# Kernel optimization log

Measured on AMD Instinct MI355X. Metric: run time of the kernel, lower is better.

## Reference

```python
import jax, jax.numpy as jnp
import numpy as np

DIM = 1024
HEAD_NUM = 8
D_HEAD = DIM // HEAD_NUM
B, S = 4, 2048


def setup_inputs() -> dict:
    key = jax.random.key(0)
    ks = jax.random.split(key, 7)
    scale = 0.02
    return {
        "Q": jax.random.normal(ks[0], (B, S, DIM), dtype=jnp.float32),
        "K": jax.random.normal(ks[1], (B, S, DIM), dtype=jnp.float32),
        "V": jax.random.normal(ks[2], (B, S, DIM), dtype=jnp.float32),
        "W_Q": jax.random.normal(ks[3], (DIM, DIM), dtype=jnp.float32) * scale,
        "W_K": jax.random.normal(ks[4], (DIM, DIM), dtype=jnp.float32) * scale,
        "W_V": jax.random.normal(ks[5], (DIM, DIM), dtype=jnp.float32) * scale,
        "W_O": jax.random.normal(ks[6], (DIM, DIM), dtype=jnp.float32) * scale,
    }


def reference(Q, K, V, W_Q, W_K, W_V, W_O):
    # torch nn.Linear(bias=False): y = x @ W.T
    b, s, d = Q.shape
    h, dh = HEAD_NUM, d // HEAD_NUM

    def proj_split(x, W):
        # split_head: tensor_split along feature dim into h contiguous chunks,
        # stack at dim 1 -> [b, h, s, dh]; equivalent to reshape+transpose.
        y = jnp.einsum('bsd,ed->bse', x, W)
        return y.reshape(b, s, h, dh).transpose(0, 2, 1, 3)

    q = proj_split(Q, W_Q)  # [b,h,s,dh]
    k = proj_split(K, W_K)
    v = proj_split(V, W_V)

    scores = jnp.einsum('bhqd,bhkd->bhqk', q, k) / jnp.sqrt(jnp.float32(dh))
    # FAITHFUL to original: nn.Softmax(dim=1) normalizes over the HEAD axis.
    attn = jax.nn.softmax(scores, axis=1)
    # dropout is identity in eval mode
    ctx = jnp.einsum('bhqk,bhkd->bhqd', attn, v)  # [b,h,s,dh]
    # concat_head: heads concatenated back along feature dim in order
    ctx = ctx.transpose(0, 2, 1, 3).reshape(b, s, d)
    return jnp.einsum('bsd,ed->bse', ctx, W_O)
```

## Files before the change

kernel.cpp:

```cpp
#include <hip/hip_runtime.h>
#include <math.h>
#include <stdint.h>


typedef __attribute__((ext_vector_type(8))) __bf16 bf16x8;
typedef __attribute__((ext_vector_type(4))) __bf16 bf16x4;
typedef __attribute__((ext_vector_type(4))) float  f32x4;

__device__ __forceinline__ f32x4 mfma16(bf16x8 a, bf16x8 b, f32x4 c) {
    return __builtin_amdgcn_mfma_f32_16x16x32_bf16(a, b, c, 0, 0, 0);
}

__device__ __forceinline__ void cp16(void* lds, const void* g) {
    __builtin_amdgcn_global_load_lds(
        (__attribute__((address_space(1))) void*)(void*)(const_cast<void*>(g)),
        (__attribute__((address_space(3))) void*)lds,
        16, 0, 0);
}

__global__ void cast4_f32_to_bf16(const float* __restrict__ s0, __bf16* __restrict__ d0,
                                  const float* __restrict__ s1, __bf16* __restrict__ d1,
                                  const float* __restrict__ s2, __bf16* __restrict__ d2,
                                  const float* __restrict__ s3, __bf16* __restrict__ d3,
                                  int n4) {
    const float* s = (blockIdx.y == 0) ? s0 : (blockIdx.y == 1) ? s1
                    : (blockIdx.y == 2) ? s2 : s3;
    __bf16* d = (blockIdx.y == 0) ? d0 : (blockIdx.y == 1) ? d1
               : (blockIdx.y == 2) ? d2 : d3;
    int i = blockIdx.x * blockDim.x + threadIdx.x;
    const int stride = gridDim.x * blockDim.x;
    for (; i < n4; i += stride) {
        float4 f = ((const float4*)s)[i];
        bf16x4 o;
        o[0] = (__bf16)f.x; o[1] = (__bf16)f.y; o[2] = (__bf16)f.z; o[3] = (__bf16)f.w;
        ((bf16x4*)d)[i] = o;
    }
}

__global__ void cast3_f32_to_bf16(const float* __restrict__ s0, __bf16* __restrict__ d0,
                                  const float* __restrict__ s1, __bf16* __restrict__ d1,
                                  const float* __restrict__ s2, __bf16* __restrict__ d2,
                                  int n4) {
    const float* s = (blockIdx.y == 0) ? s0 : (blockIdx.y == 1) ? s1 : s2;
    __bf16* d = (blockIdx.y == 0) ? d0 : (blockIdx.y == 1) ? d1 : d2;
    int i = blockIdx.x * blockDim.x + threadIdx.x;
    const int stride = gridDim.x * blockDim.x;
    for (; i < n4; i += stride) {
        float4 f = ((const float4*)s)[i];
        bf16x4 o;
        o[0] = (__bf16)f.x; o[1] = (__bf16)f.y; o[2] = (__bf16)f.z; o[3] = (__bf16)f.w;
        ((bf16x4*)d)[i] = o;
    }
}

template<int MODE>
__global__ __launch_bounds__(256, 2) void gemm_bt(const __bf16* __restrict__ A,
                                                  const __bf16* __restrict__ Bt,
                                                  void* __restrict__ out,
                                                  float scale)
{
    __shared__ __bf16 As[128 * 32];
    __shared__ __bf16 Bs[128 * 32];
    const int tid  = threadIdx.x;
    const int lane = tid & 63;
    const int u = lane >> 4, v = lane & 15;
    const int w = tid >> 6;
    const int wm = (w >> 1) * 64, wn = (w & 1) * 64;
    const long tM = (long)blockIdx.y * 128;
    const int  tN = blockIdx.x * 128;

    f32x4 acc[4][4];
#pragma unroll
    for (int i = 0; i < 4; ++i)
#pragma unroll
        for (int j = 0; j < 4; ++j) acc[i][j] = (f32x4){0.f, 0.f, 0.f, 0.f};

    const int c0 = tid, c1 = tid + 256;
    const int ar0 = c0 >> 2, ak0 = (c0 & 3) * 8;
    const int ar1 = c1 >> 2, ak1 = (c1 & 3) * 8;

    const __bf16* Ab = A  + tM * 1024;
    const __bf16* Bb = Bt + (long)tN * 1024;

    for (int k0 = 0; k0 < 1024; k0 += 32) {
        __syncthreads();
        cp16(&As[ar0 * 32 + ak0], Ab + (long)ar0 * 1024 + k0 + ak0);
        cp16(&As[ar1 * 32 + ak1], Ab + (long)ar1 * 1024 + k0 + ak1);
        cp16(&Bs[ar0 * 32 + ak0], Bb + (long)ar0 * 1024 + k0 + ak0);
        cp16(&Bs[ar1 * 32 + ak1], Bb + (long)ar1 * 1024 + k0 + ak1);
        __syncthreads();

        bf16x8 af[4], bfr[4];
#pragma unroll
        for (int i = 0; i < 4; ++i)
            af[i] = *(const bf16x8*)&As[(wm + i * 16 + v) * 32 + u * 8];
#pragma unroll
        for (int j = 0; j < 4; ++j)
            bfr[j] = *(const bf16x8*)&Bs[(wn + j * 16 + v) * 32 + u * 8];
#pragma unroll
        for (int i = 0; i < 4; ++i)
#pragma unroll
            for (int j = 0; j < 4; ++j)
                acc[i][j] = mfma16(af[i], bfr[j], acc[i][j]);
    }

#pragma unroll
    for (int i = 0; i < 4; ++i) {
#pragma unroll
        for (int j = 0; j < 4; ++j) {
            const long row0 = tM + wm + i * 16 + u * 4;
            const int  col  = tN + wn + j * 16 + v;
            if (MODE == 1) {
                float* o = (float*)out;
#pragma unroll
                for (int r = 0; r < 4; ++r)
                    o[(row0 + r) * 1024 + col] = acc[i][j][r];
            } else {
                __bf16* o = (__bf16*)out;
#pragma unroll
                for (int r = 0; r < 4; ++r)
                    o[(row0 + r) * 1024 + col] = (__bf16)(acc[i][j][r] * scale);
            }
        }
    }
}

__global__ __launch_bounds__(256, 2) void qkv_proj(
    const __bf16* __restrict__ xq, const __bf16* __restrict__ xk,
    const __bf16* __restrict__ xv,
    const __bf16* __restrict__ wq, const __bf16* __restrict__ wk,
    const __bf16* __restrict__ wv,
    __bf16* __restrict__ qp, __bf16* __restrict__ kp, __bf16* __restrict__ vtb,
    float qscale)
{
    __shared__ __bf16 As[128 * 32];
    __shared__ __bf16 Bs[128 * 32];
    const int z = blockIdx.z;
    const __bf16* A  = (z == 0) ? xq : (z == 1) ? xk : xv;
    const __bf16* Bt = (z == 0) ? wq : (z == 1) ? wk : wv;
    __bf16* out      = (z == 0) ? qp : (z == 1) ? kp : vtb;
    const float scale = (z == 0) ? qscale : 1.0f;

    const int tid  = threadIdx.x;
    const int lane = tid & 63;
    const int u = lane >> 4, v = lane & 15;
    const int w = tid >> 6;
    const int wm = (w >> 1) * 64, wn = (w & 1) * 64;
    const long tM = (long)blockIdx.y * 128;
    const int  tN = blockIdx.x * 128;

    f32x4 acc[4][4];
#pragma unroll
    for (int i = 0; i < 4; ++i)
#pragma unroll
        for (int j = 0; j < 4; ++j) acc[i][j] = (f32x4){0.f, 0.f, 0.f, 0.f};

    const int c0 = tid, c1 = tid + 256;
    const int ar0 = c0 >> 2, ak0 = (c0 & 3) * 8;
    const int ar1 = c1 >> 2, ak1 = (c1 & 3) * 8;

    const __bf16* Ab = A  + tM * 1024;
    const __bf16* Bb = Bt + (long)tN * 1024;

    for (int k0 = 0; k0 < 1024; k0 += 32) {
        __syncthreads();
        cp16(&As[ar0 * 32 + ak0], Ab + (long)ar0 * 1024 + k0 + ak0);
        cp16(&As[ar1 * 32 + ak1], Ab + (long)ar1 * 1024 + k0 + ak1);
        cp16(&Bs[ar0 * 32 + ak0], Bb + (long)ar0 * 1024 + k0 + ak0);
        cp16(&Bs[ar1 * 32 + ak1], Bb + (long)ar1 * 1024 + k0 + ak1);
        __syncthreads();

        bf16x8 af[4], bfr[4];
#pragma unroll
        for (int i = 0; i < 4; ++i)
            af[i] = *(const bf16x8*)&As[(wm + i * 16 + v) * 32 + u * 8];
#pragma unroll
        for (int j = 0; j < 4; ++j)
            bfr[j] = *(const bf16x8*)&Bs[(wn + j * 16 + v) * 32 + u * 8];
#pragma unroll
        for (int i = 0; i < 4; ++i)
#pragma unroll
            for (int j = 0; j < 4; ++j)
                acc[i][j] = mfma16(af[i], bfr[j], acc[i][j]);
    }

#pragma unroll
    for (int i = 0; i < 4; ++i) {
#pragma unroll
        for (int j = 0; j < 4; ++j) {
            const long row0 = tM + wm + i * 16 + u * 4;
            const int  col  = tN + wn + j * 16 + v;
            if (z < 2) {
#pragma unroll
                for (int r = 0; r < 4; ++r)
                    out[(row0 + r) * 1024 + col] = (__bf16)(acc[i][j][r] * scale);
            } else {
                const int bidx = (int)(row0 >> 11);
                const int s    = (int)(row0 & 2047);
                const int h = col >> 7, dh = col & 127;
                bf16x4 pk;
#pragma unroll
                for (int r = 0; r < 4; ++r) pk[r] = (__bf16)acc[i][j][r];
                *(bf16x4*)&out[((long)(bidx * 8 + h) * 128 + dh) * 2048 + s] = pk;
            }
        }
    }
}

__global__ __launch_bounds__(512, 2) void fused_attn(
    const __bf16* __restrict__ qp, const __bf16* __restrict__ kp,
    const __bf16* __restrict__ vt, __bf16* __restrict__ ctx)
{
    __shared__ f32x4 dbuf[8][8][64];
    __shared__ f32x4 rbuf[8][64];
    __shared__ __bf16 Pl[8][32][64];

    const int tid  = threadIdx.x;
    const int w    = tid >> 6;
    const int lane = tid & 63;
    const int u = lane >> 4, v = lane & 15;

    const int g0 = blockIdx.x;
    const int xs = g0 & 7, idx = g0 >> 3;
    const int b  = xs >> 1;
    const int qt = idx * 2 + (xs & 1);
    const int q0 = qt * 32;
    const int h  = w;

    const __bf16* Qb = qp + ((long)b * 2048 + q0) * 1024 + h * 128;
    const __bf16* Kb = kp + (long)b * 2048 * 1024 + h * 128;
    const __bf16* Vb = vt + (long)(b * 8 + h) * 128 * 2048;

    bf16x8 qf[2][4];
#pragma unroll
    for (int qj = 0; qj < 2; ++qj)
#pragma unroll
        for (int kk = 0; kk < 4; ++kk)
            qf[qj][kk] = *(const bf16x8*)&Qb[(long)(qj * 16 + v) * 1024 + kk * 32 + u * 8];

    f32x4 ctxa[8][2];
#pragma unroll
    for (int dt = 0; dt < 8; ++dt)
#pragma unroll
        for (int qj = 0; qj < 2; ++qj) ctxa[dt][qj] = (f32x4){0.f, 0.f, 0.f, 0.f};

    for (int kt = 0; kt < 2048; kt += 64) {
        f32x4 e[4][2];
#pragma unroll
        for (int ki = 0; ki < 4; ++ki)
#pragma unroll
            for (int qj = 0; qj < 2; ++qj) e[ki][qj] = (f32x4){0.f, 0.f, 0.f, 0.f};

#pragma unroll
        for (int ki = 0; ki < 4; ++ki) {
            bf16x8 kf[4];
#pragma unroll
            for (int kk = 0; kk < 4; ++kk)
                kf[kk] = *(const bf16x8*)&Kb[(long)(kt + ki * 16 + v) * 1024 + kk * 32 + u * 8];
#pragma unroll
            for (int qj = 0; qj < 2; ++qj)
#pragma unroll
                for (int kk = 0; kk < 4; ++kk)
                    e[ki][qj] = mfma16(kf[kk], qf[qj][kk], e[ki][qj]);
        }

#pragma unroll
        for (int ki = 0; ki < 4; ++ki)
#pragma unroll
            for (int qj = 0; qj < 2; ++qj)
#pragma unroll
                for (int r = 0; r < 4; ++r)
                    e[ki][qj][r] = __expf(e[ki][qj][r]);

        bf16x8 vf0[8];
#pragma unroll
        for (int dt = 0; dt < 8; ++dt)
            vf0[dt] = *(const bf16x8*)&Vb[(long)(dt * 16 + v) * 2048 + kt + u * 8];

#pragma unroll
        for (int ki = 0; ki < 4; ++ki)
#pragma unroll
            for (int qj = 0; qj < 2; ++qj)
                dbuf[w][ki * 2 + qj][lane] = e[ki][qj];
        __syncthreads();

        f32x4 d = dbuf[0][w][lane];
#pragma unroll
        for (int wp = 1; wp < 8; ++wp) {
            f32x4 t = dbuf[wp][w][lane];
#pragma unroll
            for (int r = 0; r < 4; ++r) d[r] += t[r];
        }
        f32x4 rv;
#pragma unroll
        for (int r = 0; r < 4; ++r) rv[r] = 1.0f / d[r];
        rbuf[w][lane] = rv;
        __syncthreads();

#pragma unroll
        for (int ki = 0; ki < 4; ++ki)
#pragma unroll
            for (int qj = 0; qj < 2; ++qj) {
                f32x4 rr = rbuf[ki * 2 + qj][lane];
                bf16x4 o;
#pragma unroll
                for (int r = 0; r < 4; ++r) o[r] = (__bf16)(e[ki][qj][r] * rr[r]);
                const int q  = qj * 16 + v;
                const int ch = (ki * 2 + (u >> 1)) ^ (v & 7);
                *(bf16x4*)((char*)&Pl[w][q][0] + ch * 16 + (u & 1) * 8) = o;
            }

        bf16x8 pfr[2][2];
#pragma unroll
        for (int kc = 0; kc < 2; ++kc)
#pragma unroll
            for (int qj = 0; qj < 2; ++qj) {
                const int q  = qj * 16 + v;
                const int ch = (kc * 4 + u) ^ (v & 7);
                pfr[kc][qj] = *(const bf16x8*)((const char*)&Pl[w][q][0] + ch * 16);
            }
#pragma unroll
        for (int dt = 0; dt < 8; ++dt) {
#pragma unroll
            for (int qj = 0; qj < 2; ++qj)
                ctxa[dt][qj] = mfma16(vf0[dt], pfr[0][qj], ctxa[dt][qj]);
            bf16x8 vf1 = *(const bf16x8*)&Vb[(long)(dt * 16 + v) * 2048 + kt + 32 + u * 8];
#pragma unroll
            for (int qj = 0; qj < 2; ++qj)
                ctxa[dt][qj] = mfma16(vf1, pfr[1][qj], ctxa[dt][qj]);
        }
    }

#pragma unroll
    for (int dt = 0; dt < 8; ++dt)
#pragma unroll
        for (int qj = 0; qj < 2; ++qj) {
            bf16x4 o;
#pragma unroll
            for (int r = 0; r < 4; ++r) o[r] = (__bf16)ctxa[dt][qj][r];
            *(bf16x4*)&ctx[((long)b * 2048 + q0 + qj * 16 + v) * 1024
                           + h * 128 + dt * 16 + u * 4] = o;
        }
}

extern "C" void kernel_launch(void* const* d_in, const int* in_sizes, int n_in,
                              void* d_out, int out_size, void* d_ws, size_t ws_size,
                              hipStream_t stream)
{
    const float* Q  = (const float*)d_in[0];
    const float* K  = (const float*)d_in[1];
    const float* V  = (const float*)d_in[2];
    const float* WQ = (const float*)d_in[3];
    const float* WK = (const float*)d_in[4];
    const float* WV = (const float*)d_in[5];
    const float* WO = (const float*)d_in[6];

    __bf16* ws = (__bf16*)d_ws;
    __bf16* wq = ws;
    __bf16* wk = wq + 1048576;
    __bf16* wv = wk + 1048576;
    __bf16* wo = wv + 1048576;
    __bf16* xq = wo + 1048576;
    __bf16* xk = xq + 8388608;
    __bf16* xv = xk + 8388608;
    __bf16* qp = xv + 8388608;
    __bf16* kp = qp + 8388608;
    __bf16* vt = kp + 8388608;
    __bf16* xb = vt + 8388608;

    const float qscale = 0.08838834764831845f;

    cast4_f32_to_bf16<<<dim3(256, 4), 256, 0, stream>>>(
        WQ, wq, WK, wk, WV, wv, WO, wo, 262144);
    cast3_f32_to_bf16<<<dim3(2048, 3), 256, 0, stream>>>(
        Q, xq, K, xk, V, xv, 2097152);
    qkv_proj<<<dim3(8, 64, 3), 256, 0, stream>>>(
        xq, xk, xv, wq, wk, wv, qp, kp, vt, qscale);

    fused_attn<<<256, 512, 0, stream>>>(qp, kp, vt, xb);

    gemm_bt<1><<<dim3(8, 64), 256, 0, stream>>>(xb, wo, (float*)d_out, 1.0f);
}
```

Before: 510.3 us.

## Prefetch next K tile in registers, add setprio, and remap GEMM block order

```diff
diff --git a/kernel.cpp b/kernel.cpp
--- a/kernel.cpp
+++ b/kernel.cpp
@@ -66,8 +66,9 @@
     const int u = lane >> 4, v = lane & 15;
     const int w = tid >> 6;
     const int wm = (w >> 1) * 64, wn = (w & 1) * 64;
-    const long tM = (long)blockIdx.y * 128;
-    const int  tN = blockIdx.x * 128;
+    const int bid = blockIdx.y * 8 + blockIdx.x;
+    const long tM = (long)(bid & 63) * 128;
+    const int  tN = (bid >> 6) * 128;
 
     f32x4 acc[4][4];
 #pragma unroll
@@ -146,8 +147,9 @@
     const int u = lane >> 4, v = lane & 15;
     const int w = tid >> 6;
     const int wm = (w >> 1) * 64, wn = (w & 1) * 64;
-    const long tM = (long)blockIdx.y * 128;
-    const int  tN = blockIdx.x * 128;
+    const int bid = blockIdx.y * 8 + blockIdx.x;
+    const long tM = (long)(bid & 63) * 128;
+    const int  tN = (bid >> 6) * 128;
 
     f32x4 acc[4][4];
 #pragma unroll
@@ -244,25 +246,38 @@
 #pragma unroll
         for (int qj = 0; qj < 2; ++qj) ctxa[dt][qj] = (f32x4){0.f, 0.f, 0.f, 0.f};
 
+    bf16x8 kf[4][4];
+#pragma unroll
+    for (int ki = 0; ki < 4; ++ki)
+#pragma unroll
+        for (int kk = 0; kk < 4; ++kk)
+            kf[ki][kk] = *(const bf16x8*)&Kb[(long)(ki * 16 + v) * 1024 + kk * 32 + u * 8];
+
     for (int kt = 0; kt < 2048; kt += 64) {
+        const int ktn = (kt + 64) & 2047;
+
         f32x4 e[4][2];
 #pragma unroll
         for (int ki = 0; ki < 4; ++ki)
 #pragma unroll
             for (int qj = 0; qj < 2; ++qj) e[ki][qj] = (f32x4){0.f, 0.f, 0.f, 0.f};
 
-#pragma unroll
-        for (int ki = 0; ki < 4; ++ki) {
-            bf16x8 kf[4];
+        __builtin_amdgcn_s_setprio(1);
+#pragma unroll
+        for (int ki = 0; ki < 4; ++ki)
+#pragma unroll
+            for (int qj = 0; qj < 2; ++qj)
+#pragma unroll
+                for (int kk = 0; kk < 4; ++kk)
+                    e[ki][qj] = mfma16(kf[ki][kk], qf[qj][kk], e[ki][qj]);
+        __builtin_amdgcn_s_setprio(0);
+
+#pragma unroll
+        for (int ki = 0; ki < 4; ++ki)
 #pragma unroll
             for (int kk = 0; kk < 4; ++kk)
-                kf[kk] = *(const bf16x8*)&Kb[(long)(kt + ki * 16 + v) * 1024 + kk * 32 + u * 8];
-#pragma unroll
-            for (int qj = 0; qj < 2; ++qj)
-#pragma unroll
-                for (int kk = 0; kk < 4; ++kk)
-                    e[ki][qj] = mfma16(kf[kk], qf[qj][kk], e[ki][qj]);
-        }
+                kf[ki][kk] = *(const bf16x8*)&Kb[(long)(ktn + ki * 16 + v) * 1024
+                                                 + kk * 32 + u * 8];
 
 #pragma unroll
         for (int ki = 0; ki < 4; ++ki)
@@ -319,6 +334,7 @@
                 const int ch = (kc * 4 + u) ^ (v & 7);
                 pfr[kc][qj] = *(const bf16x8*)((const char*)&Pl[w][q][0] + ch * 16);
             }
+        __builtin_amdgcn_s_setprio(1);
 #pragma unroll
         for (int dt = 0; dt < 8; ++dt) {
 #pragma unroll
@@ -329,6 +345,7 @@
             for (int qj = 0; qj < 2; ++qj)
                 ctxa[dt][qj] = mfma16(vf1, pfr[1][qj], ctxa[dt][qj]);
         }
+        __builtin_amdgcn_s_setprio(0);
     }
 
 #pragma unroll
```

Result: slower. 564.1 us (+10.5%).
